# Optimization experiments

Hardware: AMD Instinct MI355X
Metric: run time of the kernel (lower is better)

The kernel has to match this reference:

```python
import jax, jax.numpy as jnp
import numpy as np

N = 50000
IN_F = 200
OUT_F = 200
NRELA = 200
E1 = 400000
E2 = 100000
ALPHA = 0.2  # leakyrelu slope


def setup_inputs() -> dict:
    key = jax.random.key(0)
    ks = jax.random.split(key, 9)
    xav = float(np.sqrt(2.0 / (OUT_F + 2 * IN_F + NRELA))) * 1.414
    return {
        "x": jax.random.normal(ks[0], (N, IN_F), dtype=jnp.float32),
        "edge": jax.random.randint(ks[1], (2, E1), 0, N, dtype=jnp.int32),
        "edge_embed": jax.random.normal(ks[2], (E1, NRELA), dtype=jnp.float32),
        "edge_list_nhop": jax.random.randint(ks[3], (2, E2), 0, N, dtype=jnp.int32),
        "edge_embed_nhop": jax.random.normal(ks[4], (E2, NRELA), dtype=jnp.float32),
        "a": jax.random.normal(ks[5], (OUT_F, 2 * IN_F + NRELA), dtype=jnp.float32) * xav,
        "a_2": jax.random.normal(ks[6], (1, OUT_F), dtype=jnp.float32) * float(np.sqrt(2.0 / (1 + OUT_F))) * 1.414,
        "mlp_w": jax.random.normal(ks[7], (1, OUT_F), dtype=jnp.float32) * float(np.sqrt(1.0 / OUT_F)),
        "mlp_b": jnp.zeros((1,), dtype=jnp.float32),
    }


def reference(x, edge, edge_embed, edge_list_nhop, edge_embed_nhop, a, a_2, mlp_w, mlp_b):
    # concat 1-hop and n-hop edges: e [2,E], emb [E,nrela]
    e = jnp.concatenate([edge, edge_list_nhop], axis=1)
    emb = jnp.concatenate([edge_embed, edge_embed_nhop], axis=0)
    src = e[0]
    dst = e[1]
    n_edges = emb.shape[0]
    # edge_h: [E, 2*in + nrela]
    edge_h = jnp.concatenate([x[src], x[dst], emb], axis=1)
    # edge_m = a @ edge_h.T, kept as [E, out]
    edge_m = edge_h @ a.T
    # powers = -leakyrelu(a_2 @ edge_m): [E]
    powers = -jax.nn.leaky_relu(edge_m @ a_2[0], ALPHA)
    # inline MLP: tanh(Linear(edge_m)) -> [E]
    y = jnp.tanh(edge_m @ mlp_w[0] + mlp_b[0])
    powers = powers * y / n_edges
    edge_e = jnp.exp(powers)  # [E]
    n = x.shape[0]
    # segment-sum over source nodes (sparse.sum over dim=1 of coo[src,dst,:])
    e_rowsum = jax.ops.segment_sum(edge_e, src, num_segments=n)[:, None]  # [N,1]
    e_rowsum = jnp.where(e_rowsum == 0.0, 1e-12, e_rowsum)
    # weighted scatter-add of edge messages
    edge_w = edge_e[:, None] * edge_m  # [E, out]
    h_prime = jax.ops.segment_sum(edge_w, src, num_segments=n)  # [N, out]
    h_prime = h_prime / e_rowsum
    return jax.nn.elu(h_prime)  # concat=True
```

## Files before the change

kernel.cpp:

```cpp
#include <hip/hip_runtime.h>
#include <math.h>

#define NN    50000
#define FDIM  200
#define E1N   400000
#define E2N   100000
#define EN    500000

typedef __attribute__((ext_vector_type(8))) short short8;
typedef __attribute__((ext_vector_type(4))) float f32x4;

#define VALL_OFF   0
#define WALL_OFF   608
#define SCAL_OFF   1216
#define RS_OFF     201216
#define CNT_OFF    251216
#define FILL_OFF   301216
#define INCL_OFF   351216
#define BSUM_OFF   401216
#define SORT_OFF   401472
#define XB_OFF     1401472
#define AB_OFF     6401472
#define TSB_OFF    6461472

static __device__ __forceinline__ unsigned short f2bf(float f) {
    unsigned int u = __float_as_uint(f);
    unsigned int r = (u + 0x7fffu + ((u >> 16) & 1u)) >> 16;
    return (unsigned short)r;
}
static __device__ __forceinline__ float bf2f(unsigned short s) {
    return __uint_as_float((unsigned int)s << 16);
}

#define DPP_ADD(x, ctrl, rmask) \
    x += __int_as_float(__builtin_amdgcn_update_dpp(0, __float_as_int(x), ctrl, rmask, 0xf, true))

static __device__ __forceinline__ float wave_sum_bcast(float x) {
    DPP_ADD(x, 0x111, 0xf);
    DPP_ADD(x, 0x112, 0xf);
    DPP_ADD(x, 0x114, 0xf);
    DPP_ADD(x, 0x118, 0xf);
    DPP_ADD(x, 0x142, 0xa);
    DPP_ADD(x, 0x143, 0xc);
    return __int_as_float(__builtin_amdgcn_readlane(__float_as_int(x), 63));
}

static __device__ __forceinline__ float readlane_f(float v, int l) {
    return __int_as_float(__builtin_amdgcn_readlane(__float_as_int(v), l));
}

__global__ void k_coeffs(const float* __restrict__ a, const float* __restrict__ a2,
                         const float* __restrict__ mlpw,
                         float* __restrict__ vall, float* __restrict__ wall) {
    int k = blockIdx.x * blockDim.x + threadIdx.x;
    if (k >= 600) return;
    float v = 0.f, w = 0.f;
    for (int o = 0; o < FDIM; ++o) {
        float av = a[o * 600 + k];
        v += a2[o] * av;
        w += mlpw[o] * av;
    }
    vall[k] = v;
    wall[k] = w;
}

__global__ __launch_bounds__(256) void k_node_scal(const float* __restrict__ x,
                                                   const float* __restrict__ vall,
                                                   const float* __restrict__ wall,
                                                   float* __restrict__ scal,
                                                   unsigned short* __restrict__ xb) {
    __shared__ float sv[1200];
    int tid = threadIdx.x;
    for (int i = tid; i < 1200; i += 256) sv[i] = (i < 600) ? vall[i] : wall[i - 600];
    __syncthreads();
    int lane = tid & 63;
    int n = blockIdx.x * 4 + (tid >> 6);
    float ps = 0.f, pd = 0.f, qs = 0.f, qd = 0.f;
    if (lane < 50) {
        float4 xv = *(const float4*)(x + (size_t)n * FDIM + lane * 4);
        float4 v1 = *(const float4*)(sv + lane * 4);
        float4 v2 = *(const float4*)(sv + 200 + lane * 4);
        float4 w1 = *(const float4*)(sv + 600 + lane * 4);
        float4 w2 = *(const float4*)(sv + 800 + lane * 4);
        ps = xv.x * v1.x + xv.y * v1.y + xv.z * v1.z + xv.w * v1.w;
        pd = xv.x * v2.x + xv.y * v2.y + xv.z * v2.z + xv.w * v2.w;
        qs = xv.x * w1.x + xv.y * w1.y + xv.z * w1.z + xv.w * w1.w;
        qd = xv.x * w2.x + xv.y * w2.y + xv.z * w2.z + xv.w * w2.w;
        ushort4 o;
        o.x = f2bf(xv.x); o.y = f2bf(xv.y); o.z = f2bf(xv.z); o.w = f2bf(xv.w);
        *(ushort4*)(xb + (size_t)n * FDIM + lane * 4) = o;
    }
    ps = wave_sum_bcast(ps);
    pd = wave_sum_bcast(pd);
    qs = wave_sum_bcast(qs);
    qd = wave_sum_bcast(qd);
    if (lane == 0) {
        float4 r = make_float4(ps, pd, qs, qd);
        *(float4*)(scal + (size_t)n * 4) = r;
    }
}

__global__ __launch_bounds__(256) void k_cvt(const float* __restrict__ src,
                                             unsigned short* __restrict__ dst, int n4) {
    int i = blockIdx.x * 256 + threadIdx.x;
    if (i >= n4) return;
    float4 v = *(const float4*)(src + (size_t)i * 4);
    ushort4 o;
    o.x = f2bf(v.x); o.y = f2bf(v.y); o.z = f2bf(v.z); o.w = f2bf(v.w);
    *(ushort4*)(dst + (size_t)i * 4) = o;
}

__global__ __launch_bounds__(256) void k_hist(const int* __restrict__ edge,
                                              const int* __restrict__ edgenh,
                                              int* __restrict__ counts) {
    int g = blockIdx.x * 256 + threadIdx.x;
    if (g >= EN) return;
    int s = (g < E1N) ? edge[g] : edgenh[g - E1N];
    atomicAdd(counts + s, 1);
}

__global__ __launch_bounds__(256) void k_scan1(const int* __restrict__ counts,
                                               int* __restrict__ incl,
                                               int* __restrict__ bsums) {
    __shared__ int tmp[256];
    int g = blockIdx.x * 256 + threadIdx.x;
    int v = (g < NN) ? counts[g] : 0;
    tmp[threadIdx.x] = v;
    __syncthreads();
    for (int off = 1; off < 256; off <<= 1) {
        int t = (threadIdx.x >= off) ? tmp[threadIdx.x - off] : 0;
        __syncthreads();
        tmp[threadIdx.x] += t;
        __syncthreads();
    }
    if (g < NN) incl[g] = tmp[threadIdx.x];
    if (threadIdx.x == 255) bsums[blockIdx.x] = tmp[255];
}

__global__ __launch_bounds__(256) void k_scan2(int* __restrict__ bsums, int nb) {
    __shared__ int tmp[256];
    int v = (threadIdx.x < nb) ? bsums[threadIdx.x] : 0;
    tmp[threadIdx.x] = v;
    __syncthreads();
    for (int off = 1; off < 256; off <<= 1) {
        int t = (threadIdx.x >= off) ? tmp[threadIdx.x - off] : 0;
        __syncthreads();
        tmp[threadIdx.x] += t;
        __syncthreads();
    }
    if (threadIdx.x < nb) bsums[threadIdx.x] = tmp[threadIdx.x] - v;
}

__global__ __launch_bounds__(256) void k_scan3(const int* __restrict__ counts,
                                               int* __restrict__ incl,
                                               const int* __restrict__ bsums,
                                               int* __restrict__ fill) {
    int g = blockIdx.x * 256 + threadIdx.x;
    if (g >= NN) return;
    int v = incl[g] - counts[g] + bsums[blockIdx.x];
    incl[g] = v;
    fill[g] = v;
}

__global__ __launch_bounds__(256) void k_scatter(const int* __restrict__ edge,
                                                 const int* __restrict__ edgenh,
                                                 int* __restrict__ fill,
                                                 int2* __restrict__ sorted2) {
    int g = blockIdx.x * 256 + threadIdx.x;
    if (g >= EN) return;
    int s, d;
    if (g < E1N) { s = edge[g]; d = edge[E1N + g]; }
    else { s = edgenh[g - E1N]; d = edgenh[E2N + (g - E1N)]; }
    int pos = atomicAdd(fill + s, 1);
    sorted2[pos] = make_int2(g, d);
}

#define ISSUE(EV, XU, IDX) do {                                                   \
    int _e = __builtin_amdgcn_readlane(recx, (IDX));                              \
    int _d = __builtin_amdgcn_readlane(recy, (IDX));                              \
    const float* _er = (_e < E1N) ? ee + (size_t)_e * FDIM                        \
                                  : eenh + (size_t)(_e - E1N) * FDIM;             \
    if (lane < 50) {                                                              \
        EV = *(const float4*)(_er + lane * 4);                                    \
        XU = *(const ushort4*)(xb + (size_t)_d * FDIM + lane * 4);                \
    }                                                                             \
} while (0)

#define CONSUME(EV, XU, IDX) do {                                                 \
    float _pe = EV.x * v3.x + EV.y * v3.y + EV.z * v3.z + EV.w * v3.w;            \
    float _qe = EV.x * w3.x + EV.y * w3.y + EV.z * w3.z + EV.w * w3.w;            \
    _pe = wave_sum_bcast(_pe);                                                    \
    _qe = wave_sum_bcast(_qe);                                                    \
    float _sdy = readlane_f(sdy, (IDX));                                          \
    float _sdw = readlane_f(sdw, (IDX));                                          \
    float _z1 = scx + _sdy + _pe;                                                 \
    float _z2 = scz + _sdw + _qe + mb;                                            \
    float _l = _z1 > 0.f ? _z1 : 0.2f * _z1;                                      \
    float _e2 = __expf(2.f * _z2);                                                \
    float _t = 1.f - 2.f * __builtin_amdgcn_rcpf(_e2 + 1.f);                      \
    float _w = __expf(_l * _t * (-1.f / (float)EN));                              \
    _w = ((IDX) < m) ? _w : 0.f;                                                  \
    rs += _w;                                                                     \
    float _x0 = bf2f(XU.x), _x1 = bf2f(XU.y), _x2 = bf2f(XU.z), _x3 = bf2f(XU.w); \
    accx0 += _w * _x0; accx1 += _w * _x1; accx2 += _w * _x2; accx3 += _w * _x3;   \
    acce0 += _w * EV.x; acce1 += _w * EV.y; acce2 += _w * EV.z; acce3 += _w * EV.w; \
} while (0)

__global__ __launch_bounds__(256) void k_csr(const int2* __restrict__ sorted2,
                                             const int* __restrict__ offs,
                                             const int* __restrict__ counts,
                                             const float* __restrict__ ee,
                                             const float* __restrict__ eenh,
                                             const unsigned short* __restrict__ xb,
                                             const float* __restrict__ vall,
                                             const float* __restrict__ wall,
                                             const float* __restrict__ scal,
                                             const float* __restrict__ mlpb,
                                             float* __restrict__ rowsum,
                                             unsigned short* __restrict__ Tsb) {
    int tid = threadIdx.x, lane = tid & 63;
    int n = blockIdx.x * 4 + (tid >> 6);
    float4 v3 = make_float4(0, 0, 0, 0), w3 = v3;
    if (lane < 50) {
        v3 = *(const float4*)(vall + 400 + lane * 4);
        w3 = *(const float4*)(wall + 400 + lane * 4);
    }
    float scx = scal[(size_t)n * 4 + 0];
    float scz = scal[(size_t)n * 4 + 2];
    float mb = mlpb[0];
    int beg = offs[n], cnt = counts[n];
    float accx0 = 0, accx1 = 0, accx2 = 0, accx3 = 0;
    float acce0 = 0, acce1 = 0, acce2 = 0, acce3 = 0;
    float rs = 0.f;

    for (int c0 = 0; c0 < cnt; c0 += 64) {
        int m = cnt - c0; if (m > 64) m = 64;
        int recx = 0, recy = 0;
        float sdy = 0.f, sdw = 0.f;
        if (lane < m) {
            int2 rr = sorted2[beg + c0 + lane];
            recx = rr.x; recy = rr.y;
            sdy = scal[(size_t)rr.y * 4 + 1];
            sdw = scal[(size_t)rr.y * 4 + 3];
        }
        int m4 = (m + 3) & ~3;
        float4 ev0 = make_float4(0,0,0,0), ev1 = ev0, ev2 = ev0, ev3 = ev0;
        ushort4 xu0 = {0,0,0,0}, xu1 = xu0, xu2 = xu0, xu3 = xu0;
        ISSUE(ev0, xu0, 0);
        ISSUE(ev1, xu1, 1);
        ISSUE(ev2, xu2, 2);
        ISSUE(ev3, xu3, 3);
        for (int i = 0; i < m4; i += 4) {
            CONSUME(ev0, xu0, i + 0); if (i + 4 < m4) ISSUE(ev0, xu0, i + 4);
            CONSUME(ev1, xu1, i + 1); if (i + 5 < m4) ISSUE(ev1, xu1, i + 5);
            CONSUME(ev2, xu2, i + 2); if (i + 6 < m4) ISSUE(ev2, xu2, i + 6);
            CONSUME(ev3, xu3, i + 3); if (i + 7 < m4) ISSUE(ev3, xu3, i + 7);
        }
    }

    if (lane == 0) rowsum[n] = rs;
    float inv = (cnt > 0) ? __builtin_amdgcn_rcpf(rs) : 0.f;
    if (lane < 50) {
        ushort4 o1, o2;
        o1.x = f2bf(accx0 * inv); o1.y = f2bf(accx1 * inv);
        o1.z = f2bf(accx2 * inv); o1.w = f2bf(accx3 * inv);
        o2.x = f2bf(acce0 * inv); o2.y = f2bf(acce1 * inv);
        o2.z = f2bf(acce2 * inv); o2.w = f2bf(acce3 * inv);
        *(ushort4*)(Tsb + (size_t)n * 400 + lane * 4) = o1;
        *(ushort4*)(Tsb + (size_t)n * 400 + 200 + lane * 4) = o2;
    }
}

__global__ __launch_bounds__(256) void k_gemm_fused(const unsigned short* __restrict__ xb,
                                                    const unsigned short* __restrict__ tsb,
                                                    const unsigned short* __restrict__ ab,
                                                    const float* __restrict__ rowsum,
                                                    float* __restrict__ out) {
    __shared__ unsigned short Al[64][40];
    __shared__ unsigned short Bl[64][40];
    int tid = threadIdx.x, w = tid >> 6, lane = tid & 63;
    int h = blockIdx.y * 4 + blockIdx.x;
    int g = (h & 7) * 391 + (h >> 3);
    int by = g >> 2, bx = g & 3;
    f32x4 acc[4] = {};
    int r = tid >> 2, c = tid & 3;
    int arow = by * 64 + r;
    int brow = bx * 64 + r;
    bool inA = arow < NN;
    bool inB = brow < 200;
    const unsigned short* aPx = xb + (size_t)arow * 200;
    const unsigned short* aPt = tsb + (size_t)arow * 400;
    const unsigned short* bP = ab + (size_t)brow * 600;
    for (int k0 = 0; k0 < 640; k0 += 32) {
        int gk = k0 + c * 8;
        uint4 av = make_uint4(0, 0, 0, 0), bv = av;
        if (gk < 200) {
            if (inA) av = *(const uint4*)(aPx + gk);
            if (inB) bv = *(const uint4*)(bP + gk);
        } else if (gk >= 224 && gk < 624) {
            if (inA) av = *(const uint4*)(aPt + (gk - 224));
            if (inB) bv = *(const uint4*)(bP + gk - 24);
        }
        *(uint4*)&Al[r][c * 8] = av;
        *(uint4*)&Bl[r][c * 8] = bv;
        __syncthreads();
        short8 af = *(short8*)&Al[w * 16 + (lane & 15)][(lane >> 4) * 8];
        #pragma unroll
        for (int ct = 0; ct < 4; ++ct) {
            short8 bf = *(short8*)&Bl[ct * 16 + (lane & 15)][(lane >> 4) * 8];
            acc[ct] = __builtin_amdgcn_mfma_f32_16x16x32_bf16(af, bf, acc[ct], 0, 0, 0);
        }
        __syncthreads();
    }
    #pragma unroll
    for (int ct = 0; ct < 4; ++ct) {
        #pragma unroll
        for (int rr = 0; rr < 4; ++rr) {
            int grow = by * 64 + w * 16 + (lane >> 4) * 4 + rr;
            int gcol = bx * 64 + ct * 16 + (lane & 15);
            if (grow < NN && gcol < 200) {
                float rsv = rowsum[grow];
                float hh = acc[ct][rr];
                float o = (rsv == 0.f) ? 0.f : (hh > 0.f ? hh : expm1f(hh));
                out[(size_t)grow * 200 + gcol] = o;
            }
        }
    }
}

extern "C" void kernel_launch(void* const* d_in, const int* in_sizes, int n_in,
                              void* d_out, int out_size, void* d_ws, size_t ws_size,
                              hipStream_t stream) {
    const float* x      = (const float*)d_in[0];
    const int*   edge   = (const int*)d_in[1];
    const float* ee     = (const float*)d_in[2];
    const int*   edgenh = (const int*)d_in[3];
    const float* eenh   = (const float*)d_in[4];
    const float* a      = (const float*)d_in[5];
    const float* a2     = (const float*)d_in[6];
    const float* mlpw   = (const float*)d_in[7];
    const float* mlpb   = (const float*)d_in[8];

    float* ws = (float*)d_ws;
    float* vall   = ws + VALL_OFF;
    float* wall   = ws + WALL_OFF;
    float* scal   = ws + SCAL_OFF;
    float* rowsum = ws + RS_OFF;
    int*   counts = (int*)(ws + CNT_OFF);
    int*   fill   = (int*)(ws + FILL_OFF);
    int*   incl   = (int*)(ws + INCL_OFF);
    int*   bsums  = (int*)(ws + BSUM_OFF);
    int2*  sorted2 = (int2*)(ws + SORT_OFF);
    unsigned short* xb  = (unsigned short*)(ws + XB_OFF);
    unsigned short* ab  = (unsigned short*)(ws + AB_OFF);
    unsigned short* tsb = (unsigned short*)(ws + TSB_OFF);

    hipMemsetAsync(counts, 0, (size_t)(2 * NN) * sizeof(int), stream);

    k_coeffs<<<3, 256, 0, stream>>>(a, a2, mlpw, vall, wall);
    k_node_scal<<<NN / 4, 256, 0, stream>>>(x, vall, wall, scal, xb);
    k_cvt<<<(200 * 600 / 4 + 255) / 256, 256, 0, stream>>>(a, ab, 200 * 600 / 4);

    k_hist<<<(EN + 255) / 256, 256, 0, stream>>>(edge, edgenh, counts);
    int nb = (NN + 255) / 256;
    k_scan1<<<nb, 256, 0, stream>>>(counts, incl, bsums);
    k_scan2<<<1, 256, 0, stream>>>(bsums, nb);
    k_scan3<<<nb, 256, 0, stream>>>(counts, incl, bsums, fill);
    k_scatter<<<(EN + 255) / 256, 256, 0, stream>>>(edge, edgenh, fill, sorted2);

    k_csr<<<NN / 4, 256, 0, stream>>>(sorted2, incl, counts, ee, eenh, xb,
                                      vall, wall, scal, mlpb, rowsum, tsb);

    dim3 gg(4, (NN + 63) / 64);
    k_gemm_fused<<<gg, 256, 0, stream>>>(xb, tsb, ab, rowsum, (float*)d_out);
}
```

Before: 683.1 us.

## Merge prep kernels, use nontemporal edge loads, enlarge GEMM row tile

Folds the coefficient, bf16 conversion of `a` and source-histogram kernels into one launch, partitioned by block index, to cut launch overhead. Edge-embedding rows in the CSR kernel are now read with nontemporal loads so this streaming data does less cache pollution. The fused GEMM now computes 128-row tiles, two MFMA row fragments per wave, which doubles reuse of each B fragment and halves the workgroup count. A new XCD-aware mapping spreads workgroups across the 8 XCDs. The cost is more LDS and accumulator registers per workgroup.

```diff
diff --git a/kernel.cpp b/kernel.cpp
--- a/kernel.cpp
+++ b/kernel.cpp
@@ -49,19 +49,45 @@
     return __int_as_float(__builtin_amdgcn_readlane(__float_as_int(v), l));
 }
 
-__global__ void k_coeffs(const float* __restrict__ a, const float* __restrict__ a2,
-                         const float* __restrict__ mlpw,
-                         float* __restrict__ vall, float* __restrict__ wall) {
-    int k = blockIdx.x * blockDim.x + threadIdx.x;
-    if (k >= 600) return;
-    float v = 0.f, w = 0.f;
-    for (int o = 0; o < FDIM; ++o) {
-        float av = a[o * 600 + k];
-        v += a2[o] * av;
-        w += mlpw[o] * av;
-    }
-    vall[k] = v;
-    wall[k] = w;
+#define HIST_BLOCKS 1954
+#define CVT_BLOCKS  118
+__global__ __launch_bounds__(256) void k_prep(const float* __restrict__ a,
+                                              const float* __restrict__ a2,
+                                              const float* __restrict__ mlpw,
+                                              const int* __restrict__ edge,
+                                              const int* __restrict__ edgenh,
+                                              float* __restrict__ vall,
+                                              float* __restrict__ wall,
+                                              unsigned short* __restrict__ ab,
+                                              int* __restrict__ counts) {
+    int b = blockIdx.x;
+    if (b < HIST_BLOCKS) {
+        int g = b * 256 + threadIdx.x;
+        if (g < EN) {
+            int s = (g < E1N) ? edge[g] : edgenh[g - E1N];
+            atomicAdd(counts + s, 1);
+        }
+    } else if (b < HIST_BLOCKS + CVT_BLOCKS) {
+        int i = (b - HIST_BLOCKS) * 256 + threadIdx.x;
+        if (i < 30000) {
+            float4 v = *(const float4*)(a + (size_t)i * 4);
+            ushort4 o;
+            o.x = f2bf(v.x); o.y = f2bf(v.y); o.z = f2bf(v.z); o.w = f2bf(v.w);
+            *(ushort4*)(ab + (size_t)i * 4) = o;
+        }
+    } else {
+        int k = (b - HIST_BLOCKS - CVT_BLOCKS) * 256 + threadIdx.x;
+        if (k < 600) {
+            float v = 0.f, w = 0.f;
+            for (int o = 0; o < FDIM; ++o) {
+                float av = a[o * 600 + k];
+                v += a2[o] * av;
+                w += mlpw[o] * av;
+            }
+            vall[k] = v;
+            wall[k] = w;
+        }
+    }
 }
 
 __global__ __launch_bounds__(256) void k_node_scal(const float* __restrict__ x,
@@ -100,25 +126,6 @@
     }
 }
 
-__global__ __launch_bounds__(256) void k_cvt(const float* __restrict__ src,
-                                             unsigned short* __restrict__ dst, int n4) {
-    int i = blockIdx.x * 256 + threadIdx.x;
-    if (i >= n4) return;
-    float4 v = *(const float4*)(src + (size_t)i * 4);
-    ushort4 o;
-    o.x = f2bf(v.x); o.y = f2bf(v.y); o.z = f2bf(v.z); o.w = f2bf(v.w);
-    *(ushort4*)(dst + (size_t)i * 4) = o;
-}
-
-__global__ __launch_bounds__(256) void k_hist(const int* __restrict__ edge,
-                                              const int* __restrict__ edgenh,
-                                              int* __restrict__ counts) {
-    int g = blockIdx.x * 256 + threadIdx.x;
-    if (g >= EN) return;
-    int s = (g < E1N) ? edge[g] : edgenh[g - E1N];
-    atomicAdd(counts + s, 1);
-}
-
 __global__ __launch_bounds__(256) void k_scan1(const int* __restrict__ counts,
                                                int* __restrict__ incl,
                                                int* __restrict__ bsums) {
@@ -181,7 +188,8 @@
     const float* _er = (_e < E1N) ? ee + (size_t)_e * FDIM                        \
                                   : eenh + (size_t)(_e - E1N) * FDIM;             \
     if (lane < 50) {                                                              \
-        EV = *(const float4*)(_er + lane * 4);                                    \
+        f32x4 _t = __builtin_nontemporal_load((const f32x4*)(_er + lane * 4));    \
+        EV.x = _t.x; EV.y = _t.y; EV.z = _t.z; EV.w = _t.w;                       \
         XU = *(const ushort4*)(xb + (size_t)_d * FDIM + lane * 4);                \
     }                                                                             \
 } while (0)
@@ -271,58 +279,71 @@
     }
 }
 
+#define GEMM_NWG 1564
 __global__ __launch_bounds__(256) void k_gemm_fused(const unsigned short* __restrict__ xb,
                                                     const unsigned short* __restrict__ tsb,
                                                     const unsigned short* __restrict__ ab,
                                                     const float* __restrict__ rowsum,
                                                     float* __restrict__ out) {
-    __shared__ unsigned short Al[64][40];
+    __shared__ unsigned short Al[128][40];
     __shared__ unsigned short Bl[64][40];
     int tid = threadIdx.x, w = tid >> 6, lane = tid & 63;
-    int h = blockIdx.y * 4 + blockIdx.x;
-    int g = (h & 7) * 391 + (h >> 3);
+    int h = blockIdx.x;
+    int xcd = h & 7, pos = h >> 3;
+    int g = (xcd < 4 ? xcd * 196 : 4 * 196 + (xcd - 4) * 195) + pos;
     int by = g >> 2, bx = g & 3;
-    f32x4 acc[4] = {};
+    f32x4 acc[2][4] = {};
     int r = tid >> 2, c = tid & 3;
-    int arow = by * 64 + r;
+    int arow0 = by * 128 + r;
+    int arow1 = arow0 + 64;
     int brow = bx * 64 + r;
-    bool inA = arow < NN;
+    bool inA0 = arow0 < NN, inA1 = arow1 < NN;
     bool inB = brow < 200;
-    const unsigned short* aPx = xb + (size_t)arow * 200;
-    const unsigned short* aPt = tsb + (size_t)arow * 400;
+    const unsigned short* aPx0 = xb + (size_t)arow0 * 200;
+    const unsigned short* aPt0 = tsb + (size_t)arow0 * 400;
+    const unsigned short* aPx1 = xb + (size_t)arow1 * 200;
+    const unsigned short* aPt1 = tsb + (size_t)arow1 * 400;
     const unsigned short* bP = ab + (size_t)brow * 600;
     for (int k0 = 0; k0 < 640; k0 += 32) {
         int gk = k0 + c * 8;
-        uint4 av = make_uint4(0, 0, 0, 0), bv = av;
+        uint4 av0 = make_uint4(0, 0, 0, 0), av1 = av0, bv = av0;
         if (gk < 200) {
-            if (inA) av = *(const uint4*)(aPx + gk);
-            if (inB) bv = *(const uint4*)(bP + gk);
+            if (inA0) av0 = *(const uint4*)(aPx0 + gk);
+            if (inA1) av1 = *(const uint4*)(aPx1 + gk);
+            if (inB)  bv  = *(const uint4*)(bP + gk);
         } else if (gk >= 224 && gk < 624) {
-            if (inA) av = *(const uint4*)(aPt + (gk - 224));
-            if (inB) bv = *(const uint4*)(bP + gk - 24);
-        }
-        *(uint4*)&Al[r][c * 8] = av;
+            if (inA0) av0 = *(const uint4*)(aPt0 + (gk - 224));
+            if (inA1) av1 = *(const uint4*)(aPt1 + (gk - 224));
+            if (inB)  bv  = *(const uint4*)(bP + gk - 24);
+        }
+        *(uint4*)&Al[r][c * 8] = av0;
+        *(uint4*)&Al[r + 64][c * 8] = av1;
         *(uint4*)&Bl[r][c * 8] = bv;
         __syncthreads();
-        short8 af = *(short8*)&Al[w * 16 + (lane & 15)][(lane >> 4) * 8];
+        short8 af0 = *(short8*)&Al[w * 32 + (lane & 15)][(lane >> 4) * 8];
+        short8 af1 = *(short8*)&Al[w * 32 + 16 + (lane & 15)][(lane >> 4) * 8];
         #pragma unroll
         for (int ct = 0; ct < 4; ++ct) {
             short8 bf = *(short8*)&Bl[ct * 16 + (lane & 15)][(lane >> 4) * 8];
-            acc[ct] = __builtin_amdgcn_mfma_f32_16x16x32_bf16(af, bf, acc[ct], 0, 0, 0);
+            acc[0][ct] = __builtin_amdgcn_mfma_f32_16x16x32_bf16(af0, bf, acc[0][ct], 0, 0, 0);
+            acc[1][ct] = __builtin_amdgcn_mfma_f32_16x16x32_bf16(af1, bf, acc[1][ct], 0, 0, 0);
         }
         __syncthreads();
     }
     #pragma unroll
-    for (int ct = 0; ct < 4; ++ct) {
+    for (int m = 0; m < 2; ++m) {
         #pragma unroll
-        for (int rr = 0; rr < 4; ++rr) {
-            int grow = by * 64 + w * 16 + (lane >> 4) * 4 + rr;
-            int gcol = bx * 64 + ct * 16 + (lane & 15);
-            if (grow < NN && gcol < 200) {
-                float rsv = rowsum[grow];
-                float hh = acc[ct][rr];
-                float o = (rsv == 0.f) ? 0.f : (hh > 0.f ? hh : expm1f(hh));
-                out[(size_t)grow * 200 + gcol] = o;
+        for (int ct = 0; ct < 4; ++ct) {
+            #pragma unroll
+            for (int rr = 0; rr < 4; ++rr) {
+                int grow = by * 128 + w * 32 + m * 16 + (lane >> 4) * 4 + rr;
+                int gcol = bx * 64 + ct * 16 + (lane & 15);
+                if (grow < NN && gcol < 200) {
+                    float rsv = rowsum[grow];
+                    float hh = acc[m][ct][rr];
+                    float o = (rsv == 0.f) ? 0.f : (hh > 0.f ? hh : expm1f(hh));
+                    out[(size_t)grow * 200 + gcol] = o;
+                }
             }
         }
     }
@@ -357,11 +378,10 @@
 
     hipMemsetAsync(counts, 0, (size_t)(2 * NN) * sizeof(int), stream);
 
-    k_coeffs<<<3, 256, 0, stream>>>(a, a2, mlpw, vall, wall);
+    k_prep<<<HIST_BLOCKS + CVT_BLOCKS + 3, 256, 0, stream>>>(a, a2, mlpw, edge, edgenh,
+                                                             vall, wall, ab, counts);
     k_node_scal<<<NN / 4, 256, 0, stream>>>(x, vall, wall, scal, xb);
-    k_cvt<<<(200 * 600 / 4 + 255) / 256, 256, 0, stream>>>(a, ab, 200 * 600 / 4);
-
-    k_hist<<<(EN + 255) / 256, 256, 0, stream>>>(edge, edgenh, counts);
+
     int nb = (NN + 255) / 256;
     k_scan1<<<nb, 256, 0, stream>>>(counts, incl, bsums);
     k_scan2<<<1, 256, 0, stream>>>(bsums, nb);
@@ -371,6 +391,5 @@
     k_csr<<<NN / 4, 256, 0, stream>>>(sorted2, incl, counts, ee, eenh, xb,
                                       vall, wall, scal, mlpb, rowsum, tsb);
 
-    dim3 gg(4, (NN + 63) / 64);
-    k_gemm_fused<<<gg, 256, 0, stream>>>(xb, tsb, ab, rowsum, (float*)d_out);
-}
+    k_gemm_fused<<<GEMM_NWG, 256, 0, stream>>>(xb, tsb, ab, rowsum, (float*)d_out);
+}
```

New measurement: 666.2 us. -2.5%, faster.
